# Performance work log

Hardware: AMD Instinct MI355X
Metric: run time of the kernel (lower is better)

Reference implementation:

```python
import jax, jax.numpy as jnp
import numpy as np

B, T = 16, 8192
L, RC, DC, SC, EC, E, NC = 16, 32, 32, 256, 256, 100, 256


def conv1d(x, w, b, dilation=1):
    # x: [B, Cin, T], w: [Cout, Cin, K], b: [Cout]
    y = jax.lax.conv_general_dilated(
        x, w, window_strides=(1,), padding='VALID',
        rhs_dilation=(dilation,), dimension_numbers=('NCH', 'OIH', 'NCH'))
    return y + b[None, :, None]


def setup_inputs() -> dict:
    key = jax.random.key(0)
    ks = jax.random.split(key, 32)
    n = lambda k, shp: (jax.random.normal(k, shp) * 0.1).astype(jnp.float32)
    return dict(
        tokens=jax.random.randint(ks[0], (B, T), 0, NC),
        emb=n(ks[1], (NC, E)),
        init_w=n(ks[2], (RC, E, 1)), init_b=n(ks[3], (RC,)),
        dil_w=n(ks[4], (L, DC, RC, 2)), dil_b=n(ks[5], (L, DC)),
        filt_w=n(ks[6], (L, DC, DC, 2)), filt_b=n(ks[7], (L, DC)),
        gate_w=n(ks[8], (L, DC, DC, 2)), gate_b=n(ks[9], (L, DC)),
        res_w=n(ks[10], (L, RC, DC, 1)), res_b=n(ks[11], (L, RC)),
        skip_w=n(ks[12], (L, SC, DC, 1)), skip_b=n(ks[13], (L, SC)),
        end1_w=n(ks[14], (EC, SC, 1)), end1_b=n(ks[15], (EC,)),
        end2_w=n(ks[16], (EC, EC, 1)), end2_b=n(ks[17], (EC,)),
        fc1_w=n(ks[18], (128, 256)), fc1_b=n(ks[19], (128,)),
        fc2_w=n(ks[20], (128, 128)), fc2_b=n(ks[21], (128,)),
        fc3_w=n(ks[22], (64, 128)), fc3_b=n(ks[23], (64,)),
        fc4_w=n(ks[24], (NC, 64)), fc4_b=n(ks[25], (NC,)),
    )


def reference(tokens, emb, init_w, init_b, dil_w, dil_b, filt_w, filt_b,
              gate_w, gate_b, res_w, res_b, skip_w, skip_b,
              end1_w, end1_b, end2_w, end2_b,
              fc1_w, fc1_b, fc2_w, fc2_b, fc3_w, fc3_b, fc4_w, fc4_b):
    x = emb[tokens]                     # [B, T, E]
    x = jnp.transpose(x, (0, 2, 1))     # [B, E, T]
    x = conv1d(x, init_w, init_b)       # [B, RC, T]
    skip = None
    for i in range(L):
        d = 2 ** (i % 4)                # dilation resets each block of 4 layers
        xp = jnp.pad(x, ((0, 0), (0, 0), (d + 1, 0)))        # left pad d+1
        residual = conv1d(xp, dil_w[i], dil_b[i], dilation=d)  # [B, DC, T+1]
        f = jnp.tanh(conv1d(residual, filt_w[i], filt_b[i]))   # [B, DC, T]
        g = jax.nn.sigmoid(conv1d(residual, gate_w[i], gate_b[i]))
        x = f * g
        skip = conv1d(x, skip_w[i], skip_b[i])   # overwritten each layer (source bug, kept faithful)
        x = conv1d(x, res_w[i], res_b[i]) + residual[:, :, :-1]
    h = jax.nn.relu(conv1d(jax.nn.relu(skip), end1_w, end1_b))
    h = conv1d(h, end2_w, end2_b)       # [B, EC, T]
    h = h[:, :, -1]                     # [B, 256] last timestep only
    h = jax.nn.relu(h @ fc1_w.T + fc1_b)
    h = jax.nn.relu(h @ fc2_w.T + fc2_b)
    h = jax.nn.relu(h @ fc3_w.T + fc3_b)
    out = h @ fc4_w.T + fc4_b           # [B, NC]
    return out
```

## Files before the change

### kernel.cpp

```cpp
#include <hip/hip_runtime.h>


#define BB 16
#define TT 8192
#define LL 16
#define W0 77
#define NT 256

typedef __attribute__((ext_vector_type(8)))  short short8;
typedef __attribute__((ext_vector_type(16))) float float16;
typedef __attribute__((ext_vector_type(2)))  unsigned uv2;

#define MFMA_B16(a, b, c) __builtin_amdgcn_mfma_f32_32x32x16_bf16(a, b, c, 0, 0, 0)

__device__ __forceinline__ short f2bs(float f) {
  union { float ff; unsigned u; } v; v.ff = f;
  unsigned u = v.u;
  return (short)((u + 0x7FFFu + ((u >> 16) & 1u)) >> 16);
}
__device__ __forceinline__ float b2f(short h) {
  union { unsigned u; float f; } v;
  v.u = ((unsigned)(unsigned short)h) << 16; return v.f;
}
__device__ __forceinline__ unsigned cvtpk(float lo, float hi) {
  unsigned r;
  asm("v_cvt_pk_bf16_f32 %0, %1, %2" : "=v"(r) : "v"(lo), "v"(hi));
  return r;
}
__device__ __forceinline__ short8 mk8(unsigned a, unsigned b, unsigned c, unsigned d) {
  union { unsigned u[4]; short8 s; } z;
  z.u[0] = a; z.u[1] = b; z.u[2] = c; z.u[3] = d; return z.s;
}
__device__ __forceinline__ float u2f(unsigned u) {
  union { unsigned x; float f; } z; z.x = u; return z.f;
}

__device__ __forceinline__ float dpp_add(float x, const int ctrl_sel) {
  int xi = __float_as_int(x);
  int m;
  if (ctrl_sel == 0)      m = __builtin_amdgcn_update_dpp(0, xi, 0xB1,  0xF, 0xF, true);
  else if (ctrl_sel == 1) m = __builtin_amdgcn_update_dpp(0, xi, 0x4E,  0xF, 0xF, true);
  else if (ctrl_sel == 2) m = __builtin_amdgcn_update_dpp(0, xi, 0x124, 0xF, 0xF, true);
  else if (ctrl_sel == 3) m = __builtin_amdgcn_update_dpp(0, xi, 0x128, 0xF, 0xF, true);
  else                    m = __builtin_amdgcn_update_dpp(0, xi, 0x141, 0xF, 0xF, true);
  return x + __int_as_float(m);
}
__device__ __forceinline__ float row16_sum(float x, bool dpp) {
  if (dpp) {
    x = dpp_add(x, 0); x = dpp_add(x, 1); x = dpp_add(x, 2); x = dpp_add(x, 3);
  } else {
    #pragma unroll
    for (int d2 = 1; d2 < 16; d2 <<= 1) x += __shfl_xor(x, d2);
  }
  return x;
}
__device__ __forceinline__ float row8_sum(float x, bool dpp) {
  if (dpp) {
    x = dpp_add(x, 0); x = dpp_add(x, 1); x = dpp_add(x, 4);
  } else {
    #pragma unroll
    for (int d2 = 1; d2 < 8; d2 <<= 1) x += __shfl_xor(x, d2);
  }
  return x;
}

__device__ __forceinline__ void asmb(const unsigned* own, const unsigned* cr,
                                     int kh, unsigned* o) {
  #pragma unroll
  for (int h = 0; h < 2; h++) {
    o[4*h+0] = kh ? cr[4*h+2] : own[4*h+0];
    o[4*h+1] = kh ? cr[4*h+3] : own[4*h+1];
    o[4*h+2] = kh ? own[4*h+2] : cr[4*h+0];
    o[4*h+3] = kh ? own[4*h+3] : cr[4*h+1];
  }
}

__device__ __forceinline__ void exch(unsigned* o, int kh, int lx32, int mode) {
  if (mode < 2) {
    #pragma unroll
    for (int h = 0; h < 2; h++)
      #pragma unroll
      for (int j = 0; j < 2; j++) {
        unsigned A = o[4*h+j], C = o[4*h+2+j];
        uv2 r = __builtin_amdgcn_permlane32_swap(A, C, false, false);
        o[4*h+j]   = (mode == 0) ? r[0] : r[1];
        o[4*h+2+j] = (mode == 0) ? r[1] : r[0];
      }
  } else {
    unsigned cr[8];
    #pragma unroll
    for (int q = 0; q < 8; q++) cr[q] = (unsigned)__shfl((int)o[q], lx32);
    unsigned t[8];
    asmb(o, cr, kh, t);
    #pragma unroll
    for (int q = 0; q < 8; q++) o[q] = t[q];
  }
}

__device__ __forceinline__ void afrag2(const short* src, int row, int kh, short8* out) {
  out[0] = *(const short8*)&src[row * 32 + 8 * kh];
  out[1] = *(const short8*)&src[row * 32 + 16 + 8 * kh];
}

__device__ __forceinline__ void ldrow(const short* xb, int row, int kh, unsigned* w8) {
  #pragma unroll
  for (int h = 0; h < 2; h++) {
    short8 v = *(const short8*)&xb[row * 32 + 16 * h + 8 * kh];
    union { short8 s; unsigned u[4]; } z; z.s = v;
    #pragma unroll
    for (int s = 0; s < 4; s++) w8[4 * h + s] = z.u[s];
  }
}

__device__ __forceinline__ void load_chunk(
    int li, int cid, float* pf,
    const float* dil_w, const float* filt_w, const float* gate_w, const float* res_w)
{
  int mat = cid >> 7;
  int h = (cid >> 6) & 1, ln = cid & 63;
  int n = ln & 31, k2 = ln >> 5;
  int base = (li * 32 + n) * 32 + 16 * h + 8 * k2;
  if (mat == 6) {
    const float* p = res_w + base;
    #pragma unroll
    for (int j = 0; j < 8; j++) pf[j] = p[j];
  } else {
    const float* w = (mat < 2) ? dil_w : (mat < 4) ? filt_w : gate_w;
    const float* p = w + base * 2 + (mat & 1);
    #pragma unroll
    for (int j = 0; j < 8; j++) pf[j] = p[2 * j];
  }
}

__device__ __forceinline__ void stage_layer(
    int li, int ptid, short* dst, float* bdst,
    const float* dil_w, const float* filt_w, const float* gate_w, const float* res_w,
    const float* dil_b, const float* filt_b, const float* gate_b, const float* res_b)
{
  float pf[5][8];
  #pragma unroll
  for (int q = 0; q < 5; q++) {
    int c = ptid + q * 192;
    if (c < 896) load_chunk(li, c, pf[q], dil_w, filt_w, gate_w, res_w);
  }
  #pragma unroll
  for (int q = 0; q < 5; q++) {
    int c = ptid + q * 192;
    if (c < 896) {
      short8 v;
      #pragma unroll
      for (int j = 0; j < 8; j++) v[j] = f2bs(pf[q][j]);
      *(short8*)&dst[c * 8] = v;
    }
  }
  for (int t2 = ptid; t2 < 128; t2 += 192) {
    const float* bsrc = (t2 < 32) ? dil_b : (t2 < 64) ? filt_b : (t2 < 96) ? gate_b : res_b;
    bdst[t2] = bsrc[li * 32 + (t2 & 31)];
  }
}

template<int R, int K, bool RELU>
__device__ __forceinline__ void mv_stage(const float* __restrict__ W,
                                         const float* __restrict__ bias,
                                         const float* vin, float* vout,
                                         int tid, bool dpp)
{
  constexpr int J = K >> 6;
  constexpr int P = R >> 4;
  const int s = tid & 15, rb = tid >> 4;
  float4 vf[J];
  #pragma unroll
  for (int j = 0; j < J; j++) vf[j] = *(const float4*)&vin[(s + 16 * j) * 4];
  float part[P];
  #pragma unroll
  for (int p = 0; p < P; p++) {
    const float* wr = W + (rb + 16 * p) * K;
    float a = 0.f, c = 0.f;
    #pragma unroll
    for (int j = 0; j < J; j++) {
      float4 w = *(const float4*)&wr[(s + 16 * j) * 4];
      a += w.x * vf[j].x + w.y * vf[j].y;
      c += w.z * vf[j].z + w.w * vf[j].w;
    }
    part[p] = a + c;
  }
  #pragma unroll
  for (int p = 0; p < P; p++) part[p] = row16_sum(part[p], dpp);
  if (s < P) {
    float val = part[0];
    #pragma unroll
    for (int p = 1; p < P; p++) val = (s == p) ? part[p] : val;
    int ro = rb + 16 * s;
    float r2 = val + bias[ro];
    if (RELU) r2 = fmaxf(r2, 0.f);
    vout[ro] = r2;
  }
}

__global__ __launch_bounds__(NT, 1) void wavenet_kernel(
    const int* __restrict__ tokens,
    const float* __restrict__ emb,
    const float* __restrict__ init_w, const float* __restrict__ init_b,
    const float* __restrict__ dil_w,  const float* __restrict__ dil_b,
    const float* __restrict__ filt_w, const float* __restrict__ filt_b,
    const float* __restrict__ gate_w, const float* __restrict__ gate_b,
    const float* __restrict__ res_w,  const float* __restrict__ res_b,
    const float* __restrict__ skip_w, const float* __restrict__ skip_b,
    const float* __restrict__ end1_w, const float* __restrict__ end1_b,
    const float* __restrict__ end2_w, const float* __restrict__ end2_b,
    const float* __restrict__ fc1_w,  const float* __restrict__ fc1_b,
    const float* __restrict__ fc2_w,  const float* __restrict__ fc2_b,
    const float* __restrict__ fc3_w,  const float* __restrict__ fc3_b,
    const float* __restrict__ fc4_w,  const float* __restrict__ fc4_b,
    float* __restrict__ out)
{
  __shared__ __align__(16) short bfw[2][7168];
  __shared__ __align__(16) float bias2[2][128];
  __shared__ __align__(16) short xbuf[2][W0 * 32];
  __shared__ __align__(16) short pool[8624];
  __shared__ int tok[W0];
  __shared__ __align__(16) float vecA[256], vecB[256];

  short* rb = pool;
  short* xm = pool + 2432;
  short* l14w = pool;
  float* l14b = (float*)&pool[7168];

  const int tid  = threadIdx.x;
  const int lane = tid & 63;
  const int wv   = tid >> 6;
  const int m    = lane & 31;
  const int kh   = lane >> 5;
  const int b    = blockIdx.x;

  bool dpp;
  {
    float s16 = row16_sum((float)((tid & 15) + 1), true);
    float s8v = row8_sum((float)((tid & 7) + 1), true);
    dpp = (bool)__all((s16 == 136.0f) && (s8v == 36.0f));
  }

  if (tid < W0) tok[tid] = tokens[b * TT + (TT - 1 - tid)];
  __syncthreads();

  for (int cid = tid; cid < 77 * 14; cid += NT) {
    int u = cid / 14, s = cid % 14;
    const float* er = emb + tok[u] * 100 + s * 8;
    short8 v;
    if (s < 12) {
      #pragma unroll
      for (int j = 0; j < 8; j++) v[j] = f2bs(er[j]);
    } else if (s == 12) {
      #pragma unroll
      for (int j = 0; j < 4; j++) v[j] = f2bs(er[j]);
      #pragma unroll
      for (int j = 4; j < 8; j++) v[j] = 0;
    } else {
      #pragma unroll
      for (int j = 0; j < 8; j++) v[j] = 0;
    }
    *(short8*)&pool[u * 112 + s * 8] = v;
  }
  for (int cid = tid; cid < 896; cid += NT) {
    float pf[8];
    load_chunk(0, cid, pf, dil_w, filt_w, gate_w, res_w);
    short8 v;
    #pragma unroll
    for (int j = 0; j < 8; j++) v[j] = f2bs(pf[j]);
    *(short8*)&bfw[0][cid * 8] = v;
  }
  if (tid < 128) {
    const float* bsrc = (tid < 32) ? dil_b : (tid < 64) ? filt_b : (tid < 96) ? gate_b : res_b;
    bias2[0][tid] = bsrc[tid & 31];
  }
  __syncthreads();

  if (wv < 3) {
    short8 bi[7];
    #pragma unroll
    for (int s = 0; s < 7; s++) {
      const float* p = init_w + m * 100 + s * 16 + kh * 8;
      short8 v;
      if (s < 6) {
        #pragma unroll
        for (int j = 0; j < 8; j++) v[j] = f2bs(p[j]);
      } else if (kh == 0) {
        #pragma unroll
        for (int j = 0; j < 4; j++) v[j] = f2bs(p[j]);
        #pragma unroll
        for (int j = 4; j < 8; j++) v[j] = 0;
      } else {
        #pragma unroll
        for (int j = 0; j < 8; j++) v[j] = 0;
      }
      bi[s] = v;
    }
    const float binit = init_b[m];
    const int R = wv * 32;
    int u = R + m; if (u > 76) u = 76;
    float16 accA, accB;
    #pragma unroll
    for (int r = 0; r < 16; r++) { accA[r] = binit; accB[r] = 0.f; }
    #pragma unroll
    for (int s = 0; s < 7; s++) {
      short8 a = *(const short8*)&pool[u * 112 + s * 16 + kh * 8];
      if (s < 4) accA = MFMA_B16(a, bi[s], accA);
      else       accB = MFMA_B16(a, bi[s], accB);
    }
    #pragma unroll
    for (int r = 0; r < 16; r++) {
      int row = (r & 3) + 8 * (r >> 2) + 4 * kh;
      int uu = R + row;
      if (uu < W0) xbuf[0][uu * 32 + m] = f2bs(accA[r] + accB[r]);
    }
  }
  __syncthreads();

  int Win = W0;
  for (int i = 0; i < 10; i++) {
    const int d = 1 << (i & 3);
    const int Wout = Win - d - 1;
    const int T = (Wout + 31) / 31;
    const short* bw = bfw[i & 1];
    const float* bs = bias2[i & 1];
    const short* xin  = xbuf[i & 1];
    short* xout = xbuf[(i + 1) & 1];

    float pfo[4][8];
    float pbias = 0.f;
    const int nch = (tid < 128) ? 4 : 3;
    const bool oldpf = (T >= 3) && (i + 1 < LL);
    if (oldpf) {
      #pragma unroll
      for (int q = 0; q < 4; q++) {
        if (q < nch)
          load_chunk(i + 1, tid + q * NT, pfo[q], dil_w, filt_w, gate_w, res_w);
      }
      if (tid < 128) {
        const float* bsrc = (tid < 32) ? dil_b : (tid < 64) ? filt_b : (tid < 96) ? gate_b : res_b;
        pbias = bsrc[(i + 1) * 32 + (tid & 31)];
      }
    }
    const bool newpf = (T <= 2) && (i + 1 < LL) && (wv >= T);
    const int nP = NT - T * 64;
    const int ptid = tid - T * 64;
    float pfn[7][8];
    if (newpf) {
      #pragma unroll
      for (int q = 0; q < 7; q++) {
        int c = ptid + q * nP;
        if (c < 896) load_chunk(i + 1, c, pfn[q], dil_w, filt_w, gate_w, res_w);
      }
    }

    if (wv < T) {
      const int R = wv * 31;
      short8 B0[2], B1[2], BW[5][2];
      #pragma unroll
      for (int h = 0; h < 2; h++) {
        B0[h] = *(const short8*)&bw[((0 * 2 + h) * 64 + lane) * 8];
        B1[h] = *(const short8*)&bw[((1 * 2 + h) * 64 + lane) * 8];
      }
      #pragma unroll
      for (int mt = 0; mt < 5; mt++)
        #pragma unroll
        for (int h = 0; h < 2; h++)
          BW[mt][h] = *(const short8*)&bw[(((mt + 2) * 2 + h) * 64 + lane) * 8];

      int vra = R + m + d; if (vra > Win - 1) vra = Win - 1;
      int vrz = R + m;     if (vrz > Win - 1) vrz = Win - 1;
      short8 aA[2], aZ[2];
      afrag2(xin, vra, kh, aA);
      afrag2(xin, vrz, kh, aZ);
      float16 p1a, p1b;
      const float bc = bs[m];
      #pragma unroll
      for (int r = 0; r < 16; r++) { p1a[r] = bc; p1b[r] = 0.f; }
      p1a = MFMA_B16(aA[0], B0[0], p1a);
      p1a = MFMA_B16(aA[1], B0[1], p1a);
      p1b = MFMA_B16(aZ[0], B1[0], p1b);
      p1b = MFMA_B16(aZ[1], B1[1], p1b);
      #pragma unroll
      for (int r = 0; r < 16; r++) {
        int row = (r & 3) + 8 * (r >> 2) + 4 * kh;
        int vr = R + row;
        if (vr <= Wout) rb[vr * 32 + m] = f2bs(p1a[r] + p1b[r]);
      }
      asm volatile("s_waitcnt lgkmcnt(0)" ::: "memory");

      const int capA = (R + 31 < Wout) ? (R + 31) : Wout;
      int r1 = R + m + 1; if (r1 > capA) r1 = capA;
      int r0 = R + m;     if (r0 > Wout) r0 = Wout;
      short8 a1[2], a0[2];
      afrag2(rb, r1, kh, a1);
      afrag2(rb, r0, kh, a0);
      float cinit[16];
      #pragma unroll
      for (int r = 0; r < 16; r++) {
        int row = (r & 3) + 8 * (r >> 2) + 4 * kh;
        int rr = R + row + 1; if (rr > Wout) rr = Wout;
        cinit[r] = b2f(rb[rr * 32 + m]);
      }
      float16 Fa, Fb, Ga, Gb;
      const float bf = bs[32 + m], bg = bs[64 + m];
      #pragma unroll
      for (int r = 0; r < 16; r++) { Fa[r] = bf; Fb[r] = 0.f; Ga[r] = bg; Gb[r] = 0.f; }
      Fa = MFMA_B16(a1[0], BW[0][0], Fa);
      Fa = MFMA_B16(a1[1], BW[0][1], Fa);
      Fb = MFMA_B16(a0[0], BW[1][0], Fb);
      Fb = MFMA_B16(a0[1], BW[1][1], Fb);
      Ga = MFMA_B16(a1[0], BW[2][0], Ga);
      Ga = MFMA_B16(a1[1], BW[2][1], Ga);
      Gb = MFMA_B16(a0[0], BW[3][0], Gb);
      Gb = MFMA_B16(a0[1], BW[3][1], Gb);
      #pragma unroll
      for (int r = 0; r < 16; r++) {
        int row = (r & 3) + 8 * (r >> 2) + 4 * kh;
        int uf = R + row;
        if (row < 31 && uf < Wout) {
          float u = __expf(-2.f * (Fa[r] + Fb[r]));
          float v = __expf(-(Ga[r] + Gb[r]));
          float fg = (1.f - u) * __builtin_amdgcn_rcpf((1.f + u) * (1.f + v));
          xm[uf * 32 + m] = f2bs(fg);
        }
      }
      asm volatile("s_waitcnt lgkmcnt(0)" ::: "memory");

      const int capX = (R + 30 < Wout - 1) ? (R + 30) : (Wout - 1);
      int rx = R + m; if (rx > capX) rx = capX;
      short8 aX[2];
      afrag2(xm, rx, kh, aX);
      float16 accX;
      const float br = bs[96 + m];
      #pragma unroll
      for (int r = 0; r < 16; r++) accX[r] = br + cinit[r];
      accX = MFMA_B16(aX[0], BW[4][0], accX);
      accX = MFMA_B16(aX[1], BW[4][1], accX);
      #pragma unroll
      for (int r = 0; r < 16; r++) {
        int row = (r & 3) + 8 * (r >> 2) + 4 * kh;
        int uf = R + row;
        if (row < 31 && uf < Wout) xout[uf * 32 + m] = f2bs(accX[r]);
      }
    } else if (newpf) {
      short* dst = bfw[(i + 1) & 1];
      #pragma unroll
      for (int q = 0; q < 7; q++) {
        int c = ptid + q * nP;
        if (c < 896) {
          short8 v;
          #pragma unroll
          for (int j = 0; j < 8; j++) v[j] = f2bs(pfn[q][j]);
          *(short8*)&dst[c * 8] = v;
        }
      }
      for (int t2 = ptid; t2 < 128; t2 += nP) {
        const float* bsrc = (t2 < 32) ? dil_b : (t2 < 64) ? filt_b : (t2 < 96) ? gate_b : res_b;
        bias2[(i + 1) & 1][t2] = bsrc[(i + 1) * 32 + (t2 & 31)];
      }
    }

    if (oldpf) {
      short* dst = bfw[(i + 1) & 1];
      #pragma unroll
      for (int q = 0; q < 4; q++) {
        if (q < nch) {
          short8 v;
          #pragma unroll
          for (int j = 0; j < 8; j++) v[j] = f2bs(pfo[q][j]);
          *(short8*)&dst[(tid + q * NT) * 8] = v;
        }
      }
      if (tid < 128) bias2[(i + 1) & 1][tid] = pbias;
    }
    __syncthreads();
    Win = Wout;
  }

  {
    const int t31 = lane & 31;
    const int hb  = lane & 32;
    const int lx32 = lane ^ 32;
    unsigned xcur[8], e32[8], e33[8];
    int mode = 2;
    if (wv == 0) {
      const short* xb0 = xbuf[0];
      int tcl = t31 < Win - 1 ? t31 : Win - 1;
      ldrow(xb0, tcl, kh, xcur);
      ldrow(xb0, 32, kh, e32);
      ldrow(xb0, 33, kh, e33);
      {
        unsigned pa = (unsigned)lane;
        unsigned pb = 64u + (unsigned)lane;
        uv2 pr = __builtin_amdgcn_permlane32_swap(pa, pb, false, false);
        unsigned x0  = (unsigned)__shfl((int)pr[0], 0);
        unsigned x32 = (unsigned)__shfl((int)pr[0], 32);
        unsigned y0  = (unsigned)__shfl((int)pr[1], 0);
        unsigned y32 = (unsigned)__shfl((int)pr[1], 32);
        if      (x0 == 0u  && x32 == 64u && y0 == 32u && y32 == 96u) mode = 0;
        else if (y0 == 0u  && y32 == 64u && x0 == 32u && x32 == 96u) mode = 1;
      }
    }

    #pragma unroll
    for (int i = 10; i < LL; i++) {
      const int d = 1 << (i & 3);
      const int Wout = Win - d - 1;
      const short* bw = (i == 14) ? l14w : (i == 15) ? bfw[0] : bfw[i & 1];
      const float* bs = (i == 14) ? l14b : (i == 15) ? bias2[0] : bias2[i & 1];

      if (wv >= 1) {
        const int ptid = tid - 64;
        if (i == 10) {
          float pfA[5][8], pfB[5][8];
          #pragma unroll
          for (int q = 0; q < 5; q++) {
            int c = ptid + q * 192;
            if (c < 896) load_chunk(11, c, pfA[q], dil_w, filt_w, gate_w, res_w);
          }
          #pragma unroll
          for (int q = 0; q < 5; q++) {
            int c = ptid + q * 192;
            if (c < 896) load_chunk(14, c, pfB[q], dil_w, filt_w, gate_w, res_w);
          }
          #pragma unroll
          for (int q = 0; q < 5; q++) {
            int c = ptid + q * 192;
            if (c < 896) {
              short8 vA, vB;
              #pragma unroll
              for (int j = 0; j < 8; j++) { vA[j] = f2bs(pfA[q][j]); vB[j] = f2bs(pfB[q][j]); }
              *(short8*)&bfw[1][c * 8] = vA;
              *(short8*)&l14w[c * 8]   = vB;
            }
          }
          for (int t2 = ptid; t2 < 128; t2 += 192) {
            const float* bsrc = (t2 < 32) ? dil_b : (t2 < 64) ? filt_b : (t2 < 96) ? gate_b : res_b;
            bias2[1][t2] = bsrc[11 * 32 + (t2 & 31)];
            l14b[t2]     = bsrc[14 * 32 + (t2 & 31)];
          }
        } else if (i == 11) {
          stage_layer(12, ptid, bfw[0], bias2[0], dil_w, filt_w, gate_w, res_w,
                      dil_b, filt_b, gate_b, res_b);
        } else if (i == 12) {
          stage_layer(13, ptid, bfw[1], bias2[1], dil_w, filt_w, gate_w, res_w,
                      dil_b, filt_b, gate_b, res_b);
        } else if (i == 13) {
          stage_layer(15, ptid, bfw[0], bias2[0], dil_w, filt_w, gate_w, res_w,
                      dil_b, filt_b, gate_b, res_b);
        }
      }

      if (wv == 0) {
        short8 WA[7][2];
        #pragma unroll
        for (int mt = 0; mt < 7; mt++)
          #pragma unroll
          for (int h = 0; h < 2; h++)
            WA[mt][h] = *(const short8*)&bw[((mt * 2 + h) * 64 + lane) * 8];

        unsigned xd[8];
        if (i == 10) {
          int td = t31 + d;
          int ts = td > 31 ? 31 : td;
          #pragma unroll
          for (int q = 0; q < 8; q++) {
            unsigned s = (unsigned)__shfl((int)xcur[q], hb | ts);
            s = (td == 32) ? e32[q] : s;
            s = (td >= 33) ? e33[q] : s;
            xd[q] = s;
          }
        } else {
          int td = t31 + d; if (td > Win - 1) td = Win - 1;
          int srcd = hb | td;
          #pragma unroll
          for (int q = 0; q < 8; q++) xd[q] = (unsigned)__shfl((int)xcur[q], srcd);
        }
        float16 p1a, p1b;
        #pragma unroll
        for (int g = 0; g < 4; g++) {
          float4 b4 = *(const float4*)&bs[4 * kh + 8 * g];
          p1a[4*g+0] = b4.x; p1a[4*g+1] = b4.y; p1a[4*g+2] = b4.z; p1a[4*g+3] = b4.w;
          p1b[4*g+0] = 0.f;  p1b[4*g+1] = 0.f;  p1b[4*g+2] = 0.f;  p1b[4*g+3] = 0.f;
        }
        p1a = MFMA_B16(WA[1][0], mk8(xcur[0], xcur[1], xcur[2], xcur[3]), p1a);
        p1a = MFMA_B16(WA[1][1], mk8(xcur[4], xcur[5], xcur[6], xcur[7]), p1a);
        p1b = MFMA_B16(WA[0][0], mk8(xd[0], xd[1], xd[2], xd[3]), p1b);
        p1b = MFMA_B16(WA[0][1], mk8(xd[4], xd[5], xd[6], xd[7]), p1b);

        unsigned rb0w[8];
        #pragma unroll
        for (int q = 0; q < 8; q++)
          rb0w[q] = cvtpk(p1a[2 * q] + p1b[2 * q], p1a[2 * q + 1] + p1b[2 * q + 1]);
        exch(rb0w, kh, lx32, mode);
        int t1 = t31 + 1; if (t1 > Wout) t1 = Wout;
        int s1o = hb | t1;
        unsigned rb1w[8];
        #pragma unroll
        for (int q = 0; q < 8; q++) rb1w[q] = (unsigned)__shfl((int)rb0w[q], s1o);

        float16 Fa, Fb, Ga, Gb;
        #pragma unroll
        for (int g = 0; g < 4; g++) {
          float4 bF = *(const float4*)&bs[32 + 4 * kh + 8 * g];
          float4 bG = *(const float4*)&bs[64 + 4 * kh + 8 * g];
          Fa[4*g+0] = bF.x; Fa[4*g+1] = bF.y; Fa[4*g+2] = bF.z; Fa[4*g+3] = bF.w;
          Ga[4*g+0] = bG.x; Ga[4*g+1] = bG.y; Ga[4*g+2] = bG.z; Ga[4*g+3] = bG.w;
          Fb[4*g+0] = 0.f; Fb[4*g+1] = 0.f; Fb[4*g+2] = 0.f; Fb[4*g+3] = 0.f;
          Gb[4*g+0] = 0.f; Gb[4*g+1] = 0.f; Gb[4*g+2] = 0.f; Gb[4*g+3] = 0.f;
        }
        short8 RB00 = mk8(rb0w[0], rb0w[1], rb0w[2], rb0w[3]);
        short8 RB01 = mk8(rb0w[4], rb0w[5], rb0w[6], rb0w[7]);
        short8 RB10 = mk8(rb1w[0], rb1w[1], rb1w[2], rb1w[3]);
        short8 RB11 = mk8(rb1w[4], rb1w[5], rb1w[6], rb1w[7]);
        Fa = MFMA_B16(WA[3][0], RB00, Fa);
        Fa = MFMA_B16(WA[3][1], RB01, Fa);
        Ga = MFMA_B16(WA[5][0], RB00, Ga);
        Ga = MFMA_B16(WA[5][1], RB01, Ga);
        Fb = MFMA_B16(WA[2][0], RB10, Fb);
        Fb = MFMA_B16(WA[2][1], RB11, Fb);
        Gb = MFMA_B16(WA[4][0], RB10, Gb);
        Gb = MFMA_B16(WA[4][1], RB11, Gb);
        float fg[16];
        #pragma unroll
        for (int r = 0; r < 16; r++) {
          float u = __expf(-2.f * (Fa[r] + Fb[r]));
          float v = __expf(-(Ga[r] + Gb[r]));
          fg[r] = (1.f - u) * __builtin_amdgcn_rcpf((1.f + u) * (1.f + v));
        }
        unsigned wxm[8];
        #pragma unroll
        for (int q = 0; q < 8; q++) wxm[q] = cvtpk(fg[2 * q], fg[2 * q + 1]);

        if (i == LL - 1) {
          if (t31 == 0) {
            #pragma unroll
            for (int q = 0; q < 8; q++) {
              int c0 = (2 * q & 3) + 8 * (q >> 1) + 4 * kh;
              *(unsigned*)&xbuf[0][c0] = wxm[q];
            }
          }
        } else {
          unsigned x1[8];
          #pragma unroll
          for (int q = 0; q < 8; q++) x1[q] = rb1w[q];
          exch(x1, kh, lx32, mode);
          unsigned xmw[8];
          #pragma unroll
          for (int q = 0; q < 8; q++) xmw[q] = wxm[q];
          exch(xmw, kh, lx32, mode);
          float16 accX;
          #pragma unroll
          for (int g = 0; g < 4; g++) {
            float4 bR = *(const float4*)&bs[96 + 4 * kh + 8 * g];
            #pragma unroll
            for (int j = 0; j < 4; j++) {
              int r = 4 * g + j;
              unsigned w = x1[r >> 1];
              float rv = (r & 1) ? u2f(w & 0xFFFF0000u) : u2f(w << 16);
              accX[r] = ((const float*)&bR)[j] + rv;
            }
          }
          accX = MFMA_B16(WA[6][0], mk8(xmw[0], xmw[1], xmw[2], xmw[3]), accX);
          accX = MFMA_B16(WA[6][1], mk8(xmw[4], xmw[5], xmw[6], xmw[7]), accX);
          #pragma unroll
          for (int q = 0; q < 8; q++) xcur[q] = cvtpk(accX[2 * q], accX[2 * q + 1]);
          exch(xcur, kh, lx32, mode);
        }
      }
      if (i <= 13) __syncthreads();
      Win = Wout;
    }
  }
  __syncthreads();

  {
    const short* xmt = xbuf[0];
    const int s8 = tid & 7, rb8 = tid >> 3;
    float xv[4];
    #pragma unroll
    for (int j = 0; j < 4; j++) xv[j] = b2f(xmt[s8 * 4 + j]);
    float part[8];
    #pragma unroll
    for (int p = 0; p < 8; p++) {
      const float* wr = skip_w + (15 * 256 + rb8 + 32 * p) * 32 + s8 * 4;
      float4 w = *(const float4*)wr;
      part[p] = (w.x * xv[0] + w.y * xv[1]) + (w.z * xv[2] + w.w * xv[3]);
    }
    #pragma unroll
    for (int p = 0; p < 8; p++) part[p] = row8_sum(part[p], dpp);
    float val = part[0];
    #pragma unroll
    for (int p = 1; p < 8; p++) val = (s8 == p) ? part[p] : val;
    int ro = rb8 + 32 * s8;
    vecA[ro] = fmaxf(val + skip_b[15 * 256 + ro], 0.f);
  }
  __syncthreads();
  mv_stage<256, 256, true >(end1_w, end1_b, vecA, vecB, tid, dpp);
  __syncthreads();
  mv_stage<256, 256, false>(end2_w, end2_b, vecB, vecA, tid, dpp);
  __syncthreads();
  mv_stage<128, 256, true >(fc1_w, fc1_b, vecA, vecB, tid, dpp);
  __syncthreads();
  mv_stage<128, 128, true >(fc2_w, fc2_b, vecB, vecA, tid, dpp);
  __syncthreads();
  mv_stage< 64, 128, true >(fc3_w, fc3_b, vecA, vecB, tid, dpp);
  __syncthreads();
  mv_stage<256,  64, false>(fc4_w, fc4_b, vecB, out + b * 256, tid, dpp);
}

extern "C" void kernel_launch(void* const* d_in, const int* in_sizes, int n_in,
                              void* d_out, int out_size, void* d_ws, size_t ws_size,
                              hipStream_t stream) {
  wavenet_kernel<<<BB, NT, 0, stream>>>(
      (const int*)d_in[0],    (const float*)d_in[1],  (const float*)d_in[2],  (const float*)d_in[3],
      (const float*)d_in[4],  (const float*)d_in[5],  (const float*)d_in[6],  (const float*)d_in[7],
      (const float*)d_in[8],  (const float*)d_in[9],  (const float*)d_in[10], (const float*)d_in[11],
      (const float*)d_in[12], (const float*)d_in[13], (const float*)d_in[14], (const float*)d_in[15],
      (const float*)d_in[16], (const float*)d_in[17], (const float*)d_in[18], (const float*)d_in[19],
      (const float*)d_in[20], (const float*)d_in[21], (const float*)d_in[22], (const float*)d_in[23],
      (const float*)d_in[24], (const float*)d_in[25], (float*)d_out);
}
```

Measured before the change: 195.0 us.

## Triple-buffer layer weights with two-ahead prefetch and register-resident fragments

Layer weight and bias staging goes from double to triple buffering in shared memory, so global loads run two layers ahead and the special-cased layer 11/14 staging in the tail loop is replaced by a uniform (i+2)%3 scheme. Each wave reads its MFMA B fragments for the next layer into registers (PF) during the current layer's work, so the next layer does not start with LDS reads. Bias loads in the matvec and skip stages are hoisted ahead of the reductions. This adds more LDS use and holds 14 short8 fragment registers live across the loop, which raises register pressure.

```diff
diff --git a/kernel.cpp b/kernel.cpp
--- a/kernel.cpp
+++ b/kernel.cpp
@@ -110,6 +110,14 @@
     #pragma unroll
     for (int s = 0; s < 4; s++) w8[4 * h + s] = z.u[s];
   }
+}
+
+__device__ __forceinline__ void ldfrags(const short* bw, int lane, short8 PF[7][2]) {
+  #pragma unroll
+  for (int mt = 0; mt < 7; mt++)
+    #pragma unroll
+    for (int h = 0; h < 2; h++)
+      PF[mt][h] = *(const short8*)&bw[((mt * 2 + h) * 64 + lane) * 8];
 }
 
 __device__ __forceinline__ void load_chunk(
@@ -168,6 +176,8 @@
   constexpr int J = K >> 6;
   constexpr int P = R >> 4;
   const int s = tid & 15, rb = tid >> 4;
+  const int ro = rb + 16 * (s & (P - 1));
+  const float bb = bias[ro];
   float4 vf[J];
   #pragma unroll
   for (int j = 0; j < J; j++) vf[j] = *(const float4*)&vin[(s + 16 * j) * 4];
@@ -190,8 +200,7 @@
     float val = part[0];
     #pragma unroll
     for (int p = 1; p < P; p++) val = (s == p) ? part[p] : val;
-    int ro = rb + 16 * s;
-    float r2 = val + bias[ro];
+    float r2 = val + bb;
     if (RELU) r2 = fmaxf(r2, 0.f);
     vout[ro] = r2;
   }
@@ -214,8 +223,8 @@
     const float* __restrict__ fc4_w,  const float* __restrict__ fc4_b,
     float* __restrict__ out)
 {
-  __shared__ __align__(16) short bfw[2][7168];
-  __shared__ __align__(16) float bias2[2][128];
+  __shared__ __align__(16) short bfw[3][7168];
+  __shared__ __align__(16) float bias2[3][128];
   __shared__ __align__(16) short xbuf[2][W0 * 32];
   __shared__ __align__(16) short pool[8624];
   __shared__ int tok[W0];
@@ -223,8 +232,6 @@
 
   short* rb = pool;
   short* xm = pool + 2432;
-  short* l14w = pool;
-  float* l14b = (float*)&pool[7168];
 
   const int tid  = threadIdx.x;
   const int lane = tid & 63;
@@ -233,6 +240,8 @@
   const int kh   = lane >> 5;
   const int b    = blockIdx.x;
 
+  short8 PF[7][2];
+
   bool dpp;
   {
     float s16 = row16_sum((float)((tid & 15) + 1), true);
@@ -261,17 +270,20 @@
     }
     *(short8*)&pool[u * 112 + s * 8] = v;
   }
-  for (int cid = tid; cid < 896; cid += NT) {
+  for (int cid = tid; cid < 1792; cid += NT) {
+    int li = (cid >= 896) ? 1 : 0;
+    int c = cid - 896 * li;
     float pf[8];
-    load_chunk(0, cid, pf, dil_w, filt_w, gate_w, res_w);
+    load_chunk(li, c, pf, dil_w, filt_w, gate_w, res_w);
     short8 v;
     #pragma unroll
     for (int j = 0; j < 8; j++) v[j] = f2bs(pf[j]);
-    *(short8*)&bfw[0][cid * 8] = v;
+    *(short8*)&bfw[li][c * 8] = v;
   }
   if (tid < 128) {
     const float* bsrc = (tid < 32) ? dil_b : (tid < 64) ? filt_b : (tid < 96) ? gate_b : res_b;
     bias2[0][tid] = bsrc[tid & 31];
+    bias2[1][tid] = bsrc[32 + (tid & 31)];
   }
   __syncthreads();
 
@@ -307,6 +319,7 @@
       if (s < 4) accA = MFMA_B16(a, bi[s], accA);
       else       accB = MFMA_B16(a, bi[s], accB);
     }
+    ldfrags(bfw[0], lane, PF);
     #pragma unroll
     for (int r = 0; r < 16; r++) {
       int row = (r & 3) + 8 * (r >> 2) + 4 * kh;
@@ -321,27 +334,26 @@
     const int d = 1 << (i & 3);
     const int Wout = Win - d - 1;
     const int T = (Wout + 31) / 31;
-    const short* bw = bfw[i & 1];
-    const float* bs = bias2[i & 1];
+    const float* bs = bias2[i % 3];
     const short* xin  = xbuf[i & 1];
     short* xout = xbuf[(i + 1) & 1];
 
     float pfo[4][8];
     float pbias = 0.f;
     const int nch = (tid < 128) ? 4 : 3;
-    const bool oldpf = (T >= 3) && (i + 1 < LL);
+    const bool oldpf = (T >= 3);
     if (oldpf) {
       #pragma unroll
       for (int q = 0; q < 4; q++) {
         if (q < nch)
-          load_chunk(i + 1, tid + q * NT, pfo[q], dil_w, filt_w, gate_w, res_w);
+          load_chunk(i + 2, tid + q * NT, pfo[q], dil_w, filt_w, gate_w, res_w);
       }
       if (tid < 128) {
         const float* bsrc = (tid < 32) ? dil_b : (tid < 64) ? filt_b : (tid < 96) ? gate_b : res_b;
-        pbias = bsrc[(i + 1) * 32 + (tid & 31)];
-      }
-    }
-    const bool newpf = (T <= 2) && (i + 1 < LL) && (wv >= T);
+        pbias = bsrc[(i + 2) * 32 + (tid & 31)];
+      }
+    }
+    const bool newpf = (T <= 2) && (wv >= T);
     const int nP = NT - T * 64;
     const int ptid = tid - T * 64;
     float pfn[7][8];
@@ -349,7 +361,7 @@
       #pragma unroll
       for (int q = 0; q < 7; q++) {
         int c = ptid + q * nP;
-        if (c < 896) load_chunk(i + 1, c, pfn[q], dil_w, filt_w, gate_w, res_w);
+        if (c < 896) load_chunk(i + 2, c, pfn[q], dil_w, filt_w, gate_w, res_w);
       }
     }
 
@@ -357,15 +369,11 @@
       const int R = wv * 31;
       short8 B0[2], B1[2], BW[5][2];
       #pragma unroll
-      for (int h = 0; h < 2; h++) {
-        B0[h] = *(const short8*)&bw[((0 * 2 + h) * 64 + lane) * 8];
-        B1[h] = *(const short8*)&bw[((1 * 2 + h) * 64 + lane) * 8];
-      }
+      for (int h = 0; h < 2; h++) { B0[h] = PF[0][h]; B1[h] = PF[1][h]; }
       #pragma unroll
       for (int mt = 0; mt < 5; mt++)
         #pragma unroll
-        for (int h = 0; h < 2; h++)
-          BW[mt][h] = *(const short8*)&bw[(((mt + 2) * 2 + h) * 64 + lane) * 8];
+        for (int h = 0; h < 2; h++) BW[mt][h] = PF[mt + 2][h];
 
       int vra = R + m + d; if (vra > Win - 1) vra = Win - 1;
       int vrz = R + m;     if (vrz > Win - 1) vrz = Win - 1;
@@ -430,6 +438,7 @@
       int rx = R + m; if (rx > capX) rx = capX;
       short8 aX[2];
       afrag2(xm, rx, kh, aX);
+      ldfrags(bfw[(i + 1) % 3], lane, PF);
       float16 accX;
       const float br = bs[96 + m];
       #pragma unroll
@@ -443,7 +452,7 @@
         if (row < 31 && uf < Wout) xout[uf * 32 + m] = f2bs(accX[r]);
       }
     } else if (newpf) {
-      short* dst = bfw[(i + 1) & 1];
+      short* dst = bfw[(i + 2) % 3];
       #pragma unroll
       for (int q = 0; q < 7; q++) {
         int c = ptid + q * nP;
@@ -456,12 +465,12 @@
       }
       for (int t2 = ptid; t2 < 128; t2 += nP) {
         const float* bsrc = (t2 < 32) ? dil_b : (t2 < 64) ? filt_b : (t2 < 96) ? gate_b : res_b;
-        bias2[(i + 1) & 1][t2] = bsrc[(i + 1) * 32 + (t2 & 31)];
+        bias2[(i + 2) % 3][t2] = bsrc[(i + 2) * 32 + (t2 & 31)];
       }
     }
 
     if (oldpf) {
-      short* dst = bfw[(i + 1) & 1];
+      short* dst = bfw[(i + 2) % 3];
       #pragma unroll
       for (int q = 0; q < 4; q++) {
         if (q < nch) {
@@ -471,7 +480,7 @@
           *(short8*)&dst[(tid + q * NT) * 8] = v;
         }
       }
-      if (tid < 128) bias2[(i + 1) & 1][tid] = pbias;
+      if (tid < 128) bias2[(i + 2) % 3][tid] = pbias;
     }
     __syncthreads();
     Win = Wout;
@@ -506,49 +515,12 @@
     for (int i = 10; i < LL; i++) {
       const int d = 1 << (i & 3);
       const int Wout = Win - d - 1;
-      const short* bw = (i == 14) ? l14w : (i == 15) ? bfw[0] : bfw[i & 1];
-      const float* bs = (i == 14) ? l14b : (i == 15) ? bias2[0] : bias2[i & 1];
-
-      if (wv >= 1) {
+      const float* bs = bias2[i % 3];
+
+      if (wv >= 1 && i <= 13) {
         const int ptid = tid - 64;
-        if (i == 10) {
-          float pfA[5][8], pfB[5][8];
-          #pragma unroll
-          for (int q = 0; q < 5; q++) {
-            int c = ptid + q * 192;
-            if (c < 896) load_chunk(11, c, pfA[q], dil_w, filt_w, gate_w, res_w);
-          }
-          #pragma unroll
-          for (int q = 0; q < 5; q++) {
-            int c = ptid + q * 192;
-            if (c < 896) load_chunk(14, c, pfB[q], dil_w, filt_w, gate_w, res_w);
-          }
-          #pragma unroll
-          for (int q = 0; q < 5; q++) {
-            int c = ptid + q * 192;
-            if (c < 896) {
-              short8 vA, vB;
-              #pragma unroll
-              for (int j = 0; j < 8; j++) { vA[j] = f2bs(pfA[q][j]); vB[j] = f2bs(pfB[q][j]); }
-              *(short8*)&bfw[1][c * 8] = vA;
-              *(short8*)&l14w[c * 8]   = vB;
-            }
-          }
-          for (int t2 = ptid; t2 < 128; t2 += 192) {
-            const float* bsrc = (t2 < 32) ? dil_b : (t2 < 64) ? filt_b : (t2 < 96) ? gate_b : res_b;
-            bias2[1][t2] = bsrc[11 * 32 + (t2 & 31)];
-            l14b[t2]     = bsrc[14 * 32 + (t2 & 31)];
-          }
-        } else if (i == 11) {
-          stage_layer(12, ptid, bfw[0], bias2[0], dil_w, filt_w, gate_w, res_w,
-                      dil_b, filt_b, gate_b, res_b);
-        } else if (i == 12) {
-          stage_layer(13, ptid, bfw[1], bias2[1], dil_w, filt_w, gate_w, res_w,
-                      dil_b, filt_b, gate_b, res_b);
-        } else if (i == 13) {
-          stage_layer(15, ptid, bfw[0], bias2[0], dil_w, filt_w, gate_w, res_w,
-                      dil_b, filt_b, gate_b, res_b);
-        }
+        stage_layer(i + 2, ptid, bfw[(i + 2) % 3], bias2[(i + 2) % 3],
+                    dil_w, filt_w, gate_w, res_w, dil_b, filt_b, gate_b, res_b);
       }
 
       if (wv == 0) {
@@ -556,8 +528,7 @@
         #pragma unroll
         for (int mt = 0; mt < 7; mt++)
           #pragma unroll
-          for (int h = 0; h < 2; h++)
-            WA[mt][h] = *(const short8*)&bw[((mt * 2 + h) * 64 + lane) * 8];
+          for (int h = 0; h < 2; h++) WA[mt][h] = PF[mt][h];
 
         unsigned xd[8];
         if (i == 10) {
@@ -632,6 +603,8 @@
         #pragma unroll
         for (int q = 0; q < 8; q++) wxm[q] = cvtpk(fg[2 * q], fg[2 * q + 1]);
 
+        if (i < LL - 1) ldfrags(bfw[(i + 1) % 3], lane, PF);
+
         if (i == LL - 1) {
           if (t31 == 0) {
             #pragma unroll
@@ -677,6 +650,8 @@
   {
     const short* xmt = xbuf[0];
     const int s8 = tid & 7, rb8 = tid >> 3;
+    const int ro = rb8 + 32 * s8;
+    const float sb = skip_b[15 * 256 + ro];
     float xv[4];
     #pragma unroll
     for (int j = 0; j < 4; j++) xv[j] = b2f(xmt[s8 * 4 + j]);
@@ -692,8 +667,7 @@
     float val = part[0];
     #pragma unroll
     for (int p = 1; p < 8; p++) val = (s8 == p) ? part[p] : val;
-    int ro = rb8 + 32 * s8;
-    vecA[ro] = fmaxf(val + skip_b[15 * 256 + ro], 0.f);
+    vecA[ro] = fmaxf(val + sb, 0.f);
   }
   __syncthreads();
   mv_stage<256, 256, true >(end1_w, end1_b, vecA, vecB, tid, dpp);
```

After: 194.2 us. About the same (-0.4%).
